# Performance work log

Measured on AMD Instinct MI355X. Metric: run time of the kernel, lower is better.

The kernel has to match this reference:

```python
import jax, jax.numpy as jnp
import numpy as np

DIM = 384
WS = 7
NH = 12
N = WS * WS
B_ = 4096
HEAD_DIM = DIM // NH
SCALE = HEAD_DIM ** (-0.5)


def _relative_position_index(ws: int) -> np.ndarray:
    coords = np.stack(np.meshgrid(np.arange(ws), np.arange(ws), indexing='ij'))  # [2,ws,ws]
    cf = coords.reshape(2, -1)  # [2, N]
    rel = cf[:, :, None] - cf[:, None, :]  # [2, N, N]
    rel = rel.transpose(1, 2, 0).copy()
    rel[:, :, 0] += ws - 1
    rel[:, :, 1] += ws - 1
    rel[:, :, 0] *= 2 * ws - 1
    return rel.sum(-1).astype(np.int32)  # [N, N]


def setup_inputs() -> dict:
    key = jax.random.key(0)
    ks = jax.random.split(key, 6)
    x = jax.random.normal(ks[0], (B_, N, DIM), dtype=jnp.float32)
    qkv_w = jax.random.normal(ks[1], (3 * DIM, DIM), dtype=jnp.float32) * 0.02
    qkv_b = jnp.zeros((3 * DIM,), dtype=jnp.float32)
    proj_w = jax.random.normal(ks[2], (DIM, DIM), dtype=jnp.float32) * 0.02
    proj_b = jnp.zeros((DIM,), dtype=jnp.float32)
    bias_table = jax.random.normal(ks[3], ((2 * WS - 1) * (2 * WS - 1), NH), dtype=jnp.float32) * 0.02
    rel_index = jnp.asarray(_relative_position_index(WS))  # [N, N] int32
    return {"x": x, "qkv_w": qkv_w, "qkv_b": qkv_b, "proj_w": proj_w,
            "proj_b": proj_b, "bias_table": bias_table, "rel_index": rel_index}


def reference(x, qkv_w, qkv_b, proj_w, proj_b, bias_table, rel_index):
    b, n, c = x.shape
    qkv = x @ qkv_w.T + qkv_b  # [B_, N, 3C]
    qkv = qkv.reshape(b, n, 3, NH, HEAD_DIM).transpose(2, 0, 3, 1, 4)  # [3, B_, H, N, hd]
    q, k, v = qkv[0], qkv[1], qkv[2]
    q = q * SCALE
    attn = jnp.einsum('bhnd,bhmd->bhnm', q, k)  # [B_, H, N, N]
    # relative position bias gather: [N*N] -> [N, N, H] -> [H, N, N]
    bias = bias_table[rel_index.reshape(-1)].reshape(n, n, NH).transpose(2, 0, 1)
    attn = attn + bias[None]
    attn = jax.nn.softmax(attn, axis=-1)
    out = jnp.einsum('bhnm,bhmd->bhnd', attn, v)  # [B_, H, N, hd]
    out = out.transpose(0, 2, 1, 3).reshape(b, n, c)
    return out @ proj_w.T + proj_b
```

## Files before the change

kernel.cpp:

```cpp
#include <hip/hip_runtime.h>
#include <stdint.h>
#include <stddef.h>

#define DIM_C    384
#define NHEADS   12
#define SEQ      49
#define HEADD    32
#define NWIN     4096
#define MTOT     (NWIN * SEQ)
#define QKV_N    (3 * DIM_C)
#define ATTN_SCALE 0.17677669529663687f

typedef __bf16 bf16_t;
typedef __bf16 bf16x8 __attribute__((ext_vector_type(8)));
typedef __bf16 bf16x4 __attribute__((ext_vector_type(4)));
typedef float  f32x4  __attribute__((ext_vector_type(4)));

static_assert(sizeof(bf16x8) == 16, "bf16x8 must be 16B");

#define QKV_BYTES   ((size_t)MTOT * QKV_N * 2)
#define AOUT_BYTES  ((size_t)MTOT * DIM_C * 2)
#define BIAS_ELEMS  (NHEADS * SEQ * SEQ)

__global__ void bias_expand_kernel(const float* __restrict__ table,
                                   const int* __restrict__ rel,
                                   float* __restrict__ bias_full) {
    int i = blockIdx.x * 256 + threadIdx.x;
    if (i < BIAS_ELEMS) {
        int h  = i / (SEQ * SEQ);
        int mn = i % (SEQ * SEQ);
        bias_full[i] = table[rel[mn] * NHEADS + h];
    }
}

template <bool A_BF16, bool OUT_BF16>
__global__ __launch_bounds__(256) void gemm_kernel(
    const void* __restrict__ Av, const float* __restrict__ B,
    const float* __restrict__ bias, void* __restrict__ Cv, int ldc) {
    __shared__ bf16_t As[128 * 40];
    __shared__ bf16_t Bs[128 * 40];

    const int tid  = threadIdx.x;
    const int lane = tid & 63;
    const int wave = tid >> 6;
    const int l15  = lane & 15;
    const int quad = lane >> 4;
    const int wm = (wave >> 1) * 64;
    const int wn = (wave & 1) * 64;
    const size_t m0 = (size_t)blockIdx.y * 128;
    const int    n0 = blockIdx.x * 128;

    f32x4 acc[4][4];
#pragma unroll
    for (int i = 0; i < 4; i++)
#pragma unroll
        for (int j = 0; j < 4; j++) acc[i][j] = f32x4{0.f, 0.f, 0.f, 0.f};

    for (int kt = 0; kt < DIM_C / 32; ++kt) {
        const int k0 = kt * 32;
        __syncthreads();
        if constexpr (A_BF16) {
            const bf16_t* A = (const bf16_t*)Av;
#pragma unroll
            for (int i = 0; i < 2; i++) {
                int c = tid + i * 256;
                int row = c >> 2, kq = c & 3;
                bf16x8 v = *(const bf16x8*)(A + (m0 + row) * DIM_C + k0 + kq * 8);
                *(bf16x8*)(&As[row * 40 + kq * 8]) = v;
            }
        } else {
            const float* A = (const float*)Av;
#pragma unroll
            for (int i = 0; i < 4; i++) {
                int c = tid + i * 256;
                int row = c >> 3, kq = c & 7;
                float4 v = *(const float4*)(A + (m0 + row) * DIM_C + k0 + kq * 4);
                bf16x4 t;
                t[0] = (bf16_t)v.x; t[1] = (bf16_t)v.y;
                t[2] = (bf16_t)v.z; t[3] = (bf16_t)v.w;
                *(bf16x4*)(&As[row * 40 + kq * 4]) = t;
            }
        }
        {
#pragma unroll
            for (int i = 0; i < 4; i++) {
                int c = tid + i * 256;
                int row = c >> 3, kq = c & 7;
                float4 v = *(const float4*)(B + (size_t)(n0 + row) * DIM_C + k0 + kq * 4);
                bf16x4 t;
                t[0] = (bf16_t)v.x; t[1] = (bf16_t)v.y;
                t[2] = (bf16_t)v.z; t[3] = (bf16_t)v.w;
                *(bf16x4*)(&Bs[row * 40 + kq * 4]) = t;
            }
        }
        __syncthreads();
        bf16x8 af[4], bfr[4];
#pragma unroll
        for (int mi = 0; mi < 4; mi++)
            af[mi] = *(const bf16x8*)(&As[(wm + mi * 16 + l15) * 40 + quad * 8]);
#pragma unroll
        for (int ni = 0; ni < 4; ni++)
            bfr[ni] = *(const bf16x8*)(&Bs[(wn + ni * 16 + l15) * 40 + quad * 8]);
#pragma unroll
        for (int mi = 0; mi < 4; mi++)
#pragma unroll
            for (int ni = 0; ni < 4; ni++)
                acc[mi][ni] = __builtin_amdgcn_mfma_f32_16x16x32_bf16(
                    af[mi], bfr[ni], acc[mi][ni], 0, 0, 0);
    }
#pragma unroll
    for (int mi = 0; mi < 4; mi++) {
#pragma unroll
        for (int ni = 0; ni < 4; ni++) {
            int col = n0 + wn + ni * 16 + l15;
            float bc = bias[col];
#pragma unroll
            for (int r = 0; r < 4; r++) {
                size_t row = m0 + wm + mi * 16 + quad * 4 + r;
                float v = acc[mi][ni][r] + bc;
                if constexpr (OUT_BF16)
                    ((bf16_t*)Cv)[row * (size_t)ldc + col] = (bf16_t)v;
                else
                    ((float*)Cv)[row * (size_t)ldc + col] = v;
            }
        }
    }
}

__global__ __launch_bounds__(256) void attn_kernel(
    const bf16_t* __restrict__ qkv, const float* __restrict__ bias_full,
    bf16_t* __restrict__ aout) {
    __shared__ bf16_t Ps[4][64 * 72];

    const int b    = blockIdx.x;
    const int lane = threadIdx.x & 63;
    const int wave = threadIdx.x >> 6;
    const int l15  = lane & 15;
    const int quad = lane >> 4;
    const bf16_t* base = qkv + (size_t)b * SEQ * QKV_N;
    bf16_t* ps = &Ps[wave][0];

#pragma unroll 1
    for (int hi = 0; hi < 3; ++hi) {
        const int h = wave * 3 + hi;
        bf16x8 qf[4], kf[4];
#pragma unroll
        for (int mi = 0; mi < 4; mi++) {
            int row = mi * 16 + l15;
            if (row < SEQ) {
                qf[mi] = *(const bf16x8*)(base + (size_t)row * QKV_N + h * HEADD + quad * 8);
                kf[mi] = *(const bf16x8*)(base + (size_t)row * QKV_N + DIM_C + h * HEADD + quad * 8);
            } else {
                bf16x8 z;
#pragma unroll
                for (int j = 0; j < 8; j++) z[j] = (bf16_t)0.f;
                qf[mi] = z; kf[mi] = z;
            }
        }
        f32x4 S[4][4];
#pragma unroll
        for (int mi = 0; mi < 4; mi++)
#pragma unroll
            for (int ni = 0; ni < 4; ni++)
                S[mi][ni] = __builtin_amdgcn_mfma_f32_16x16x32_bf16(
                    qf[mi], kf[ni], f32x4{0.f, 0.f, 0.f, 0.f}, 0, 0, 0);
        const float* bh = bias_full + h * SEQ * SEQ;
#pragma unroll
        for (int mi = 0; mi < 4; mi++)
#pragma unroll
            for (int r = 0; r < 4; r++) {
                int m = mi * 16 + quad * 4 + r;
#pragma unroll
                for (int ni = 0; ni < 4; ni++) {
                    int n = ni * 16 + l15;
                    float s = S[mi][ni][r];
                    s = (m < SEQ && n < SEQ) ? s * ATTN_SCALE + bh[m * SEQ + n] : -1e30f;
                    S[mi][ni][r] = s;
                }
            }
#pragma unroll
        for (int mi = 0; mi < 4; mi++)
#pragma unroll
            for (int r = 0; r < 4; r++) {
                float mx = -1e30f;
#pragma unroll
                for (int ni = 0; ni < 4; ni++) mx = fmaxf(mx, S[mi][ni][r]);
#pragma unroll
                for (int off = 1; off < 16; off <<= 1)
                    mx = fmaxf(mx, __shfl_xor(mx, off, 64));
                float sum = 0.f;
#pragma unroll
                for (int ni = 0; ni < 4; ni++) {
                    float e = __expf(S[mi][ni][r] - mx);
                    S[mi][ni][r] = e;
                    sum += e;
                }
#pragma unroll
                for (int off = 1; off < 16; off <<= 1)
                    sum += __shfl_xor(sum, off, 64);
                float inv = 1.f / sum;
                int m = mi * 16 + quad * 4 + r;
#pragma unroll
                for (int ni = 0; ni < 4; ni++) {
                    int n = ni * 16 + l15;
                    ps[m * 72 + n] = (bf16_t)(S[mi][ni][r] * inv);
                }
            }
        bf16x8 vf[2][2];
#pragma unroll
        for (int ki = 0; ki < 2; ki++)
#pragma unroll
            for (int di = 0; di < 2; di++) {
#pragma unroll
                for (int j = 0; j < 8; j++) {
                    int k = ki * 32 + quad * 8 + j;
                    vf[ki][di][j] = (k < SEQ)
                        ? base[(size_t)k * QKV_N + 2 * DIM_C + h * HEADD + di * 16 + l15]
                        : (bf16_t)0.f;
                }
            }
        f32x4 O[4][2];
#pragma unroll
        for (int mi = 0; mi < 4; mi++)
#pragma unroll
            for (int di = 0; di < 2; di++) O[mi][di] = f32x4{0.f, 0.f, 0.f, 0.f};
#pragma unroll
        for (int mi = 0; mi < 4; mi++)
#pragma unroll
            for (int ki = 0; ki < 2; ki++) {
                bf16x8 pa = *(const bf16x8*)(ps + (mi * 16 + l15) * 72 + ki * 32 + quad * 8);
#pragma unroll
                for (int di = 0; di < 2; di++)
                    O[mi][di] = __builtin_amdgcn_mfma_f32_16x16x32_bf16(
                        pa, vf[ki][di], O[mi][di], 0, 0, 0);
            }
#pragma unroll
        for (int mi = 0; mi < 4; mi++)
#pragma unroll
            for (int di = 0; di < 2; di++)
#pragma unroll
                for (int r = 0; r < 4; r++) {
                    int m = mi * 16 + quad * 4 + r;
                    if (m < SEQ)
                        aout[((size_t)b * SEQ + m) * DIM_C + h * HEADD + di * 16 + l15] =
                            (bf16_t)O[mi][di][r];
                }
    }
}

extern "C" void kernel_launch(void* const* d_in, const int* in_sizes, int n_in,
                              void* d_out, int out_size, void* d_ws, size_t ws_size,
                              hipStream_t stream) {
    (void)in_sizes; (void)n_in; (void)out_size; (void)ws_size;
    const float* x      = (const float*)d_in[0];
    const float* qkv_w  = (const float*)d_in[1];
    const float* qkv_b  = (const float*)d_in[2];
    const float* proj_w = (const float*)d_in[3];
    const float* proj_b = (const float*)d_in[4];
    const float* btable = (const float*)d_in[5];
    const int*   rel    = (const int*)d_in[6];
    float* out = (float*)d_out;

    char* ws = (char*)d_ws;
    bf16_t* qkv       = (bf16_t*)ws;
    bf16_t* aout      = (bf16_t*)(ws + QKV_BYTES);
    float*  bias_full = (float*)(ws + QKV_BYTES + AOUT_BYTES);

    bias_expand_kernel<<<(BIAS_ELEMS + 255) / 256, 256, 0, stream>>>(btable, rel, bias_full);
    gemm_kernel<false, true><<<dim3(QKV_N / 128, MTOT / 128), 256, 0, stream>>>(
        x, qkv_w, qkv_b, qkv, QKV_N);
    attn_kernel<<<NWIN, 256, 0, stream>>>(qkv, bias_full, aout);
    gemm_kernel<true, false><<<dim3(DIM_C / 128, MTOT / 128), 256, 0, stream>>>(
        aout, proj_w, proj_b, out, DIM_C);
}
```

Baseline: 1.539 ms.

## Load full-K A tile once per block and stream pre-converted bf16 weights

```diff
diff --git a/kernel.cpp b/kernel.cpp
--- a/kernel.cpp
+++ b/kernel.cpp
@@ -10,6 +10,7 @@
 #define MTOT     (NWIN * SEQ)
 #define QKV_N    (3 * DIM_C)
 #define ATTN_SCALE 0.17677669529663687f
+#define PAD_K    392
 
 typedef __bf16 bf16_t;
 typedef __bf16 bf16x8 __attribute__((ext_vector_type(8)));
@@ -18,9 +19,23 @@
 
 static_assert(sizeof(bf16x8) == 16, "bf16x8 must be 16B");
 
-#define QKV_BYTES   ((size_t)MTOT * QKV_N * 2)
-#define AOUT_BYTES  ((size_t)MTOT * DIM_C * 2)
-#define BIAS_ELEMS  (NHEADS * SEQ * SEQ)
+#define QKV_BYTES     ((size_t)MTOT * QKV_N * 2)
+#define AOUT_BYTES    ((size_t)MTOT * DIM_C * 2)
+#define BIAS_ELEMS    (NHEADS * SEQ * SEQ)
+#define BIASF_BYTES   ((size_t)BIAS_ELEMS * 4)
+#define QKVW_BF_BYTES ((size_t)QKV_N * DIM_C * 2)
+
+__global__ void convert_f32_bf16_kernel(const float* __restrict__ src,
+                                        bf16_t* __restrict__ dst, int n4) {
+    int i = blockIdx.x * 256 + threadIdx.x;
+    if (i < n4) {
+        float4 v = ((const float4*)src)[i];
+        bf16x4 t;
+        t[0] = (bf16_t)v.x; t[1] = (bf16_t)v.y;
+        t[2] = (bf16_t)v.z; t[3] = (bf16_t)v.w;
+        ((bf16x4*)dst)[i] = t;
+    }
+}
 
 __global__ void bias_expand_kernel(const float* __restrict__ table,
                                    const int* __restrict__ rel,
@@ -33,96 +48,87 @@
     }
 }
 
-template <bool A_BF16, bool OUT_BF16>
-__global__ __launch_bounds__(256) void gemm_kernel(
-    const void* __restrict__ Av, const float* __restrict__ B,
+template <bool A_BF16, bool OUT_BF16, int NT>
+__global__ __launch_bounds__(512) void gemm_fullk_kernel(
+    const void* __restrict__ Av, const bf16_t* __restrict__ Bw,
     const float* __restrict__ bias, void* __restrict__ Cv, int ldc) {
-    __shared__ bf16_t As[128 * 40];
-    __shared__ bf16_t Bs[128 * 40];
+    __shared__ bf16_t As[128 * PAD_K];
 
     const int tid  = threadIdx.x;
     const int lane = tid & 63;
     const int wave = tid >> 6;
     const int l15  = lane & 15;
     const int quad = lane >> 4;
-    const int wm = (wave >> 1) * 64;
-    const int wn = (wave & 1) * 64;
-    const size_t m0 = (size_t)blockIdx.y * 128;
-    const int    n0 = blockIdx.x * 128;
-
-    f32x4 acc[4][4];
-#pragma unroll
-    for (int i = 0; i < 4; i++)
-#pragma unroll
-        for (int j = 0; j < 4; j++) acc[i][j] = f32x4{0.f, 0.f, 0.f, 0.f};
-
-    for (int kt = 0; kt < DIM_C / 32; ++kt) {
-        const int k0 = kt * 32;
-        __syncthreads();
+    const int wm   = (wave & 3) * 32;
+    const int wn   = (wave >> 2) * 64;
+    const size_t m0 = (size_t)blockIdx.x * 128;
+
+    {
+        const int row = tid >> 2;
+        bf16_t* dst = &As[row * PAD_K];
         if constexpr (A_BF16) {
-            const bf16_t* A = (const bf16_t*)Av;
-#pragma unroll
-            for (int i = 0; i < 2; i++) {
-                int c = tid + i * 256;
-                int row = c >> 2, kq = c & 3;
-                bf16x8 v = *(const bf16x8*)(A + (m0 + row) * DIM_C + k0 + kq * 8);
-                *(bf16x8*)(&As[row * 40 + kq * 8]) = v;
+            const bf16_t* src = (const bf16_t*)Av + (m0 + row) * DIM_C;
+#pragma unroll
+            for (int i = 0; i < 12; i++) {
+                int c = (tid & 3) + i * 4;
+                *(bf16x8*)(dst + c * 8) = *(const bf16x8*)(src + c * 8);
             }
         } else {
-            const float* A = (const float*)Av;
-#pragma unroll
-            for (int i = 0; i < 4; i++) {
-                int c = tid + i * 256;
-                int row = c >> 3, kq = c & 7;
-                float4 v = *(const float4*)(A + (m0 + row) * DIM_C + k0 + kq * 4);
+            const float* src = (const float*)Av + (m0 + row) * DIM_C;
+#pragma unroll
+            for (int i = 0; i < 24; i++) {
+                int c = (tid & 3) + i * 4;
+                float4 v = *(const float4*)(src + c * 4);
                 bf16x4 t;
                 t[0] = (bf16_t)v.x; t[1] = (bf16_t)v.y;
                 t[2] = (bf16_t)v.z; t[3] = (bf16_t)v.w;
-                *(bf16x4*)(&As[row * 40 + kq * 4]) = t;
-            }
-        }
-        {
-#pragma unroll
-            for (int i = 0; i < 4; i++) {
-                int c = tid + i * 256;
-                int row = c >> 3, kq = c & 7;
-                float4 v = *(const float4*)(B + (size_t)(n0 + row) * DIM_C + k0 + kq * 4);
-                bf16x4 t;
-                t[0] = (bf16_t)v.x; t[1] = (bf16_t)v.y;
-                t[2] = (bf16_t)v.z; t[3] = (bf16_t)v.w;
-                *(bf16x4*)(&Bs[row * 40 + kq * 4]) = t;
-            }
-        }
-        __syncthreads();
-        bf16x8 af[4], bfr[4];
-#pragma unroll
-        for (int mi = 0; mi < 4; mi++)
-            af[mi] = *(const bf16x8*)(&As[(wm + mi * 16 + l15) * 40 + quad * 8]);
-#pragma unroll
-        for (int ni = 0; ni < 4; ni++)
-            bfr[ni] = *(const bf16x8*)(&Bs[(wn + ni * 16 + l15) * 40 + quad * 8]);
-#pragma unroll
-        for (int mi = 0; mi < 4; mi++)
-#pragma unroll
-            for (int ni = 0; ni < 4; ni++)
-                acc[mi][ni] = __builtin_amdgcn_mfma_f32_16x16x32_bf16(
-                    af[mi], bfr[ni], acc[mi][ni], 0, 0, 0);
-    }
-#pragma unroll
-    for (int mi = 0; mi < 4; mi++) {
-#pragma unroll
-        for (int ni = 0; ni < 4; ni++) {
-            int col = n0 + wn + ni * 16 + l15;
-            float bc = bias[col];
-#pragma unroll
-            for (int r = 0; r < 4; r++) {
-                size_t row = m0 + wm + mi * 16 + quad * 4 + r;
-                float v = acc[mi][ni][r] + bc;
-                if constexpr (OUT_BF16)
-                    ((bf16_t*)Cv)[row * (size_t)ldc + col] = (bf16_t)v;
-                else
-                    ((float*)Cv)[row * (size_t)ldc + col] = v;
-            }
+                *(bf16x4*)(dst + c * 4) = t;
+            }
+        }
+    }
+    __syncthreads();
+
+#pragma unroll 1
+    for (int ni = 0; ni < NT; ++ni) {
+        const int n0 = ni * 128;
+        f32x4 acc[2][4];
+#pragma unroll
+        for (int mi = 0; mi < 2; mi++)
+#pragma unroll
+            for (int nj = 0; nj < 4; nj++) acc[mi][nj] = f32x4{0.f, 0.f, 0.f, 0.f};
+
+#pragma unroll
+        for (int kt = 0; kt < DIM_C / 32; ++kt) {
+            bf16x8 af[2], bfr[4];
+#pragma unroll
+            for (int mi = 0; mi < 2; mi++)
+                af[mi] = *(const bf16x8*)(&As[(wm + mi * 16 + l15) * PAD_K + kt * 32 + quad * 8]);
+#pragma unroll
+            for (int nj = 0; nj < 4; nj++)
+                bfr[nj] = *(const bf16x8*)(Bw + (size_t)(n0 + wn + nj * 16 + l15) * DIM_C + kt * 32 + quad * 8);
+#pragma unroll
+            for (int mi = 0; mi < 2; mi++)
+#pragma unroll
+                for (int nj = 0; nj < 4; nj++)
+                    acc[mi][nj] = __builtin_amdgcn_mfma_f32_16x16x32_bf16(
+                        af[mi], bfr[nj], acc[mi][nj], 0, 0, 0);
+        }
+
+#pragma unroll
+        for (int nj = 0; nj < 4; nj++) {
+            const int col = n0 + wn + nj * 16 + l15;
+            const float bc = bias[col];
+#pragma unroll
+            for (int mi = 0; mi < 2; mi++)
+#pragma unroll
+                for (int r = 0; r < 4; r++) {
+                    const size_t row = m0 + wm + mi * 16 + quad * 4 + r;
+                    float v = acc[mi][nj][r] + bc;
+                    if constexpr (OUT_BF16)
+                        ((bf16_t*)Cv)[row * (size_t)ldc + col] = (bf16_t)v;
+                    else
+                        ((float*)Cv)[row * (size_t)ldc + col] = v;
+                }
         }
     }
 }
@@ -262,14 +268,21 @@
     float* out = (float*)d_out;
 
     char* ws = (char*)d_ws;
-    bf16_t* qkv       = (bf16_t*)ws;
-    bf16_t* aout      = (bf16_t*)(ws + QKV_BYTES);
-    float*  bias_full = (float*)(ws + QKV_BYTES + AOUT_BYTES);
-
+    bf16_t* qkv        = (bf16_t*)ws;
+    bf16_t* aout       = (bf16_t*)(ws + QKV_BYTES);
+    float*  bias_full  = (float*)(ws + QKV_BYTES + AOUT_BYTES);
+    bf16_t* qkv_w_bf   = (bf16_t*)(ws + QKV_BYTES + AOUT_BYTES + BIASF_BYTES);
+    bf16_t* proj_w_bf  = (bf16_t*)(ws + QKV_BYTES + AOUT_BYTES + BIASF_BYTES + QKVW_BF_BYTES);
+
+    convert_f32_bf16_kernel<<<(QKV_N * DIM_C / 4 + 255) / 256, 256, 0, stream>>>(
+        qkv_w, qkv_w_bf, QKV_N * DIM_C / 4);
+    convert_f32_bf16_kernel<<<(DIM_C * DIM_C / 4 + 255) / 256, 256, 0, stream>>>(
+        proj_w, proj_w_bf, DIM_C * DIM_C / 4);
     bias_expand_kernel<<<(BIAS_ELEMS + 255) / 256, 256, 0, stream>>>(btable, rel, bias_full);
-    gemm_kernel<false, true><<<dim3(QKV_N / 128, MTOT / 128), 256, 0, stream>>>(
-        x, qkv_w, qkv_b, qkv, QKV_N);
+
+    gemm_fullk_kernel<false, true, QKV_N / 128><<<MTOT / 128, 512, 0, stream>>>(
+        x, qkv_w_bf, qkv_b, qkv, QKV_N);
     attn_kernel<<<NWIN, 256, 0, stream>>>(qkv, bias_full, aout);
-    gemm_kernel<true, false><<<dim3(DIM_C / 128, MTOT / 128), 256, 0, stream>>>(
-        aout, proj_w, proj_b, out, DIM_C);
-}
+    gemm_fullk_kernel<true, false, DIM_C / 128><<<MTOT / 128, 512, 0, stream>>>(
+        aout, proj_w_bf, proj_b, out, DIM_C);
+}
```

Result: slower. 1.946 ms (+26.4%).

## Pre-convert weights to bf16 and remap GEMM blocks across XCDs

Applied to the files above, without the earlier changes.

```diff
diff --git a/kernel.cpp b/kernel.cpp
--- a/kernel.cpp
+++ b/kernel.cpp
@@ -18,9 +18,23 @@
 
 static_assert(sizeof(bf16x8) == 16, "bf16x8 must be 16B");
 
-#define QKV_BYTES   ((size_t)MTOT * QKV_N * 2)
-#define AOUT_BYTES  ((size_t)MTOT * DIM_C * 2)
-#define BIAS_ELEMS  (NHEADS * SEQ * SEQ)
+#define QKV_BYTES     ((size_t)MTOT * QKV_N * 2)
+#define AOUT_BYTES    ((size_t)MTOT * DIM_C * 2)
+#define BIAS_ELEMS    (NHEADS * SEQ * SEQ)
+#define BIASF_BYTES   ((size_t)BIAS_ELEMS * 4)
+#define QKVW_BF_BYTES ((size_t)QKV_N * DIM_C * 2)
+
+__global__ void convert_f32_bf16_kernel(const float* __restrict__ src,
+                                        bf16_t* __restrict__ dst, int n4) {
+    int i = blockIdx.x * 256 + threadIdx.x;
+    if (i < n4) {
+        float4 v = ((const float4*)src)[i];
+        bf16x4 t;
+        t[0] = (bf16_t)v.x; t[1] = (bf16_t)v.y;
+        t[2] = (bf16_t)v.z; t[3] = (bf16_t)v.w;
+        ((bf16x4*)dst)[i] = t;
+    }
+}
 
 __global__ void bias_expand_kernel(const float* __restrict__ table,
                                    const int* __restrict__ rel,
@@ -33,9 +47,9 @@
     }
 }
 
-template <bool A_BF16, bool OUT_BF16>
+template <bool A_BF16, bool OUT_BF16, int NT>
 __global__ __launch_bounds__(256) void gemm_kernel(
-    const void* __restrict__ Av, const float* __restrict__ B,
+    const void* __restrict__ Av, const bf16_t* __restrict__ Bw,
     const float* __restrict__ bias, void* __restrict__ Cv, int ldc) {
     __shared__ bf16_t As[128 * 40];
     __shared__ bf16_t Bs[128 * 40];
@@ -47,8 +61,12 @@
     const int quad = lane >> 4;
     const int wm = (wave >> 1) * 64;
     const int wn = (wave & 1) * 64;
-    const size_t m0 = (size_t)blockIdx.y * 128;
-    const int    n0 = blockIdx.x * 128;
+
+    const int cpx = gridDim.x >> 3;
+    const int bid = blockIdx.x;
+    const int wid = (bid & 7) * cpx + (bid >> 3);
+    const size_t m0 = (size_t)(wid / NT) * 128;
+    const int    n0 = (wid % NT) * 128;
 
     f32x4 acc[4][4];
 #pragma unroll
@@ -83,14 +101,11 @@
         }
         {
 #pragma unroll
-            for (int i = 0; i < 4; i++) {
+            for (int i = 0; i < 2; i++) {
                 int c = tid + i * 256;
-                int row = c >> 3, kq = c & 7;
-                float4 v = *(const float4*)(B + (size_t)(n0 + row) * DIM_C + k0 + kq * 4);
-                bf16x4 t;
-                t[0] = (bf16_t)v.x; t[1] = (bf16_t)v.y;
-                t[2] = (bf16_t)v.z; t[3] = (bf16_t)v.w;
-                *(bf16x4*)(&Bs[row * 40 + kq * 4]) = t;
+                int row = c >> 2, kq = c & 3;
+                bf16x8 v = *(const bf16x8*)(Bw + (size_t)(n0 + row) * DIM_C + k0 + kq * 8);
+                *(bf16x8*)(&Bs[row * 40 + kq * 8]) = v;
             }
         }
         __syncthreads();
@@ -262,14 +277,21 @@
     float* out = (float*)d_out;
 
     char* ws = (char*)d_ws;
-    bf16_t* qkv       = (bf16_t*)ws;
-    bf16_t* aout      = (bf16_t*)(ws + QKV_BYTES);
-    float*  bias_full = (float*)(ws + QKV_BYTES + AOUT_BYTES);
-
+    bf16_t* qkv        = (bf16_t*)ws;
+    bf16_t* aout       = (bf16_t*)(ws + QKV_BYTES);
+    float*  bias_full  = (float*)(ws + QKV_BYTES + AOUT_BYTES);
+    bf16_t* qkv_w_bf   = (bf16_t*)(ws + QKV_BYTES + AOUT_BYTES + BIASF_BYTES);
+    bf16_t* proj_w_bf  = (bf16_t*)(ws + QKV_BYTES + AOUT_BYTES + BIASF_BYTES + QKVW_BF_BYTES);
+
+    convert_f32_bf16_kernel<<<(QKV_N * DIM_C / 4 + 255) / 256, 256, 0, stream>>>(
+        qkv_w, qkv_w_bf, QKV_N * DIM_C / 4);
+    convert_f32_bf16_kernel<<<(DIM_C * DIM_C / 4 + 255) / 256, 256, 0, stream>>>(
+        proj_w, proj_w_bf, DIM_C * DIM_C / 4);
     bias_expand_kernel<<<(BIAS_ELEMS + 255) / 256, 256, 0, stream>>>(btable, rel, bias_full);
-    gemm_kernel<false, true><<<dim3(QKV_N / 128, MTOT / 128), 256, 0, stream>>>(
-        x, qkv_w, qkv_b, qkv, QKV_N);
+
+    gemm_kernel<false, true, QKV_N / 128><<<(MTOT / 128) * (QKV_N / 128), 256, 0, stream>>>(
+        x, qkv_w_bf, qkv_b, qkv, QKV_N);
     attn_kernel<<<NWIN, 256, 0, stream>>>(qkv, bias_full, aout);
-    gemm_kernel<true, false><<<dim3(DIM_C / 128, MTOT / 128), 256, 0, stream>>>(
-        aout, proj_w, proj_b, out, DIM_C);
-}
+    gemm_kernel<true, false, DIM_C / 128><<<(MTOT / 128) * (DIM_C / 128), 256, 0, stream>>>(
+        aout, proj_w_bf, proj_b, out, DIM_C);
+}
```

Measured after the change: 1.476 ms. 1.04x faster.
